# Performance work log

Hardware: AMD Instinct MI355X
Metric: run time of the kernel (lower is better)

The kernel has to match this reference:

```python
import jax, jax.numpy as jnp
import numpy as np

B, N, NSAMPLE = 8, 2048, 32
D = 64          # input feature channels
C1, C2 = 64, 128  # MLP channels (channels list after +3 on input: 67 -> 64 -> 128)
RADIUS = 0.15
EPS = 1e-5


def setup_inputs() -> dict:
    key = jax.random.key(0)
    ks = jax.random.split(key, 4)
    position = jax.random.uniform(ks[0], (B, N, 3), dtype=jnp.float32)
    feature = jax.random.normal(ks[1], (B, N, D), dtype=jnp.float32)
    W1 = jax.random.normal(ks[2], (D + 3, C1), dtype=jnp.float32) * 0.05
    gamma1 = jnp.ones((C1,), jnp.float32)
    beta1 = jnp.zeros((C1,), jnp.float32)
    W2 = jax.random.normal(ks[3], (C1, C2), dtype=jnp.float32) * 0.05
    gamma2 = jnp.ones((C2,), jnp.float32)
    beta2 = jnp.zeros((C2,), jnp.float32)
    return {"position": position, "feature": feature,
            "W1": W1, "gamma1": gamma1, "beta1": beta1,
            "W2": W2, "gamma2": gamma2, "beta2": beta2}


def _ball_query(xyz, radius, nsample):
    # squared pairwise distances [B, N, N]
    sq = (jnp.sum(xyz ** 2, -1)[:, :, None]
          + jnp.sum(xyz ** 2, -1)[:, None, :]
          - 2.0 * jnp.einsum('bnc,bmc->bnm', xyz, xyz))
    n = xyz.shape[1]
    idx = jnp.where(sq > radius ** 2, n, jnp.arange(n, dtype=jnp.int32)[None, None, :])
    idx = jnp.sort(idx, axis=-1)[:, :, :nsample]            # [B, N, nsample]
    first = idx[:, :, :1]
    return jnp.where(idx == n, first, idx)                  # pad misses with first neighbor


def _gather(points, idx):
    # points [B, N, C], idx [B, S, K] -> [B, S, K, C]
    b, s, k = idx.shape
    flat = jnp.take_along_axis(points, idx.reshape(b, s * k, 1), axis=1)
    return flat.reshape(b, s, k, points.shape[-1])


def _bn_relu(x, gamma, beta, relu=True):
    # BatchNorm1d over channel dim (train-mode stats across B*N*S), per linearblock
    mean = jnp.mean(x, axis=(0, 1, 2), keepdims=True)
    var = jnp.var(x, axis=(0, 1, 2), keepdims=True)
    y = (x - mean) * jax.lax.rsqrt(var + EPS) * gamma + beta
    return jax.nn.relu(y) if relu else y


def reference(position, feature, W1, gamma1, beta1, W2, gamma2, beta2):
    b, n, _ = position.shape
    idx = _ball_query(position, RADIUS, NSAMPLE)            # [B, N, nsample]
    grouped_xyz = _gather(position, idx) - position[:, :, None, :]  # [B,N,ns,3]
    grouped_feat = _gather(feature, idx)                    # [B, N, ns, D]
    h = jnp.concatenate([grouped_xyz, grouped_feat], axis=-1)  # [B, N, ns, 3+D]
    h = _bn_relu(h @ W1, gamma1, beta1)                     # [B, N, ns, C1]
    h = _bn_relu(h @ W2, gamma2, beta2)                     # [B, N, ns, C2]
    new_feature = jnp.max(h, axis=2)                        # [B, N, C2]
    return position, new_feature
```

## Files before the change

kernel.cpp:

```cpp
#include <hip/hip_runtime.h>
#include <hip/hip_bf16.h>


#define BB 8
#define NN 2048
#define KK 32
#define DD 64
#define CC1 64
#define CC2 128
#define TOTROWS (BB*NN*KK)
#define SITES (BB*NN)
#define PSLICES 256
#define DBLOCKS 1024

typedef __bf16 bf16x8 __attribute__((ext_vector_type(8)));
typedef float  f32x4  __attribute__((ext_vector_type(4)));

__device__ __forceinline__ void lds_add(float* p, float v) {
  __hip_atomic_fetch_add(p, v, __ATOMIC_RELAXED, __HIP_MEMORY_SCOPE_WORKGROUP);
}

__global__ __launch_bounds__(1024, 1) void kQ_ball_scatter(
    const float* __restrict__ pos, int* __restrict__ idx,
    float* __restrict__ Pc, float* __restrict__ Px,
    float* __restrict__ Py, float* __restrict__ Pz,
    float* __restrict__ momP, float* __restrict__ out)
{
  __shared__ float4 P[NN];
  __shared__ unsigned int Sc[NN], Sx[NN], Sy[NN], Sz[NN];
  __shared__ int idxL[64*KK];
  __shared__ float mred[16*9];
  const int b = blockIdx.x >> 5;
  const int slice = blockIdx.x & 31;
  for (int i = threadIdx.x; i < NN; i += 1024) {
    const float* p = pos + ((size_t)b*NN + i)*3;
    float x = p[0], y = p[1], z = p[2];
    float s = __fadd_rn(__fadd_rn(__fmul_rn(x,x), __fmul_rn(y,y)), __fmul_rn(z,z));
    P[i] = make_float4(x, y, z, s);
    Sc[i] = 0u; Sx[i] = 0u; Sy[i] = 0u; Sz[i] = 0u;
  }
  __syncthreads();
  const int wave = threadIdx.x >> 6, lane = threadIdx.x & 63;
  const float R2 = (float)(0.15 * 0.15);
  const unsigned long long lt = (lane == 63) ? 0x7fffffffffffffffull
                                             : ((1ull << lane) - 1ull);
  for (int qi = wave; qi < 64; qi += 16) {
    const int q = slice*64 + qi;
    const float4 Q = P[q];
    int* ip = idx + ((size_t)b*NN + q)*KK;
    int* il = idxL + qi*KK;
    int cnt = 0, first = -1;
    for (int step = 0; step < 32; ++step) {
      float4 p = P[step*64 + lane];
      float d = __fmul_rn(Q.x, p.x);
      d = fmaf(Q.y, p.y, d);
      d = fmaf(Q.z, p.z, d);
      float sq = __fsub_rn(__fadd_rn(Q.w, p.w), __fmul_rn(2.0f, d));
      bool in = !(sq > R2);
      unsigned long long mask = __ballot(in);
      if (first < 0 && mask) first = step*64 + (int)__builtin_ctzll(mask);
      int dst = cnt + (int)__popcll(mask & lt);
      if (in && dst < KK) { ip[dst] = step*64 + lane; il[dst] = step*64 + lane; }
      cnt += (int)__popcll(mask);
      if (cnt >= KK) break;
    }
    if (lane >= cnt && lane < KK) { ip[lane] = first; il[lane] = first; }
  }
  __syncthreads();
  const int sl = threadIdx.x >> 4;
  const int kg = threadIdx.x & 15;
  const int ip0 = idxL[sl*KK];
  const float4 C = P[slice*64 + sl];
  const float FS = 4194304.0f;
  float m1x=0.f,m1y=0.f,m1z=0.f,mxx=0.f,myy=0.f,mzz=0.f,mxy=0.f,mxz=0.f,myz=0.f;
  int wt = 0;
  #pragma unroll
  for (int j = 0; j < 2; ++j) {
    const int k = kg*2 + j;
    const int m = idxL[sl*KK + k];
    const float4 Pm = P[m];
    float dx = Pm.x - C.x;
    float dy = Pm.y - C.y;
    float dz = Pm.z - C.z;
    if (k > 0 && m == ip0) {
      ++wt;
    } else {
      atomicAdd(&Sc[m], 1u);
      atomicAdd(&Sx[m], (unsigned int)__float2int_rn(dx*FS));
      atomicAdd(&Sy[m], (unsigned int)__float2int_rn(dy*FS));
      atomicAdd(&Sz[m], (unsigned int)__float2int_rn(dz*FS));
    }
    m1x += dx; m1y += dy; m1z += dz;
    mxx = fmaf(dx,dx,mxx); myy = fmaf(dy,dy,myy); mzz = fmaf(dz,dz,mzz);
    mxy = fmaf(dx,dy,mxy); mxz = fmaf(dx,dz,mxz); myz = fmaf(dy,dz,myz);
  }
  if (wt > 0) {
    const float4 P0 = P[ip0];
    float dx0 = P0.x - C.x;
    float dy0 = P0.y - C.y;
    float dz0 = P0.z - C.z;
    atomicAdd(&Sc[ip0], (unsigned int)wt);
    atomicAdd(&Sx[ip0], (unsigned int)(wt*__float2int_rn(dx0*FS)));
    atomicAdd(&Sy[ip0], (unsigned int)(wt*__float2int_rn(dy0*FS)));
    atomicAdd(&Sz[ip0], (unsigned int)(wt*__float2int_rn(dz0*FS)));
  }
  const int wv = threadIdx.x >> 6;
  float vals[9] = {m1x,m1y,m1z,mxx,myy,mzz,mxy,mxz,myz};
  #pragma unroll
  for (int i = 0; i < 9; ++i) {
    float v = vals[i];
    #pragma unroll
    for (int s = 1; s < 64; s <<= 1) v += __shfl_xor(v, s, 64);
    if (lane == 0) mred[wv*9 + i] = v;
  }
  __syncthreads();
  const float IS = 2.38418579101562500e-7f;
  float* pc = Pc + (size_t)blockIdx.x*NN;
  float* px = Px + (size_t)blockIdx.x*NN;
  float* py = Py + (size_t)blockIdx.x*NN;
  float* pz = Pz + (size_t)blockIdx.x*NN;
  for (int i = threadIdx.x; i < NN; i += 1024) {
    pc[i] = (float)Sc[i];
    px[i] = (float)(int)Sx[i] * IS;
    py[i] = (float)(int)Sy[i] * IS;
    pz[i] = (float)(int)Sz[i] * IS;
  }
  if (threadIdx.x < 9) {
    float s = 0.f;
    #pragma unroll
    for (int w2 = 0; w2 < 16; ++w2) s += mred[w2*9 + threadIdx.x];
    momP[(size_t)blockIdx.x*16 + threadIdx.x] = s;
  }
  if (threadIdx.x < 192)
    out[blockIdx.x*192 + threadIdx.x] = pos[blockIdx.x*192 + threadIdx.x];
}

__global__ __launch_bounds__(256) void kB_g(const float* __restrict__ feat,
                                            const float* __restrict__ W1,
                                            const float* __restrict__ Pc,
                                            const float* __restrict__ Px,
                                            const float* __restrict__ Py,
                                            const float* __restrict__ Pz,
                                            float* __restrict__ g,
                                            float* __restrict__ A_p)
{
  __shared__ float red[320];
  __shared__ float cntL[128], dxL[128], dyL[128], dzL[128];
  for (int i = threadIdx.x; i < 320; i += 256) red[i] = 0.f;
  const int row0B = blockIdx.x * 128;
  const int bb = row0B >> 11;
  for (int r2 = threadIdx.x; r2 < 128; r2 += 256) {
    const int m = (row0B + r2) & (NN-1);
    float s0 = 0.f, s1 = 0.f, s2 = 0.f, s3 = 0.f;
    #pragma unroll 4
    for (int q = 0; q < 32; ++q) {
      const size_t base = (size_t)(bb*32 + q)*NN + m;
      s0 += Pc[base]; s1 += Px[base]; s2 += Py[base]; s3 += Pz[base];
    }
    cntL[r2] = s0; dxL[r2] = s1; dyL[r2] = s2; dzL[r2] = s3;
  }
  __syncthreads();
  const int lane = threadIdx.x & 63;
  const int quad = lane >> 4;
  const int col  = lane & 15;
  const int gw = (blockIdx.x*256 + threadIdx.x) >> 6;

  bf16x8 Bf[2][4];
  #pragma unroll
  for (int kt = 0; kt < 2; ++kt)
    #pragma unroll
    for (int nt = 0; nt < 4; ++nt) {
      bf16x8 v;
      #pragma unroll
      for (int j = 0; j < 8; ++j)
        v[j] = (__bf16)W1[(3 + kt*32 + quad*8 + j)*CC1 + nt*16 + col];
      Bf[kt][nt] = v;
    }
  float a1[4], a2[4], a3[4], a4[4], a5[4];
  #pragma unroll
  for (int nt = 0; nt < 4; ++nt) { a1[nt]=0.f; a2[nt]=0.f; a3[nt]=0.f; a4[nt]=0.f; a5[nt]=0.f; }

  for (int t = 0; t < 2; ++t) {
    const int row0 = (gw*2 + t) * 16;
    bf16x8 Af[2];
    #pragma unroll
    for (int kt = 0; kt < 2; ++kt) {
      const float4* fp =
        (const float4*)(feat + (size_t)(row0 + col)*DD + kt*32 + quad*8);
      float4 f0 = fp[0], f1 = fp[1];
      float fv[8] = {f0.x,f0.y,f0.z,f0.w,f1.x,f1.y,f1.z,f1.w};
      bf16x8 v;
      #pragma unroll
      for (int j = 0; j < 8; ++j) v[j] = (__bf16)fv[j];
      Af[kt] = v;
    }
    float cw[4], dxw[4], dyw[4], dzw[4];
    #pragma unroll
    for (int r = 0; r < 4; ++r) {
      int rl = row0 - row0B + quad*4 + r;
      cw[r] = cntL[rl]; dxw[r] = dxL[rl]; dyw[r] = dyL[rl]; dzw[r] = dzL[rl];
    }
    #pragma unroll
    for (int nt = 0; nt < 4; ++nt) {
      f32x4 a = {0.f, 0.f, 0.f, 0.f};
      a = __builtin_amdgcn_mfma_f32_16x16x32_bf16(Af[0], Bf[0][nt], a, 0, 0, 0);
      a = __builtin_amdgcn_mfma_f32_16x16x32_bf16(Af[1], Bf[1][nt], a, 0, 0, 0);
      #pragma unroll
      for (int r = 0; r < 4; ++r) {
        float v = a[r];
        g[(size_t)(row0 + quad*4 + r)*CC1 + nt*16 + col] = v;
        float cv = cw[r]*v;
        a1[nt] += cv; a2[nt] = fmaf(cv, v, a2[nt]);
        a3[nt] = fmaf(dxw[r], v, a3[nt]);
        a4[nt] = fmaf(dyw[r], v, a4[nt]);
        a5[nt] = fmaf(dzw[r], v, a5[nt]);
      }
    }
  }
  #pragma unroll
  for (int nt = 0; nt < 4; ++nt) {
    float v1=a1[nt], v2=a2[nt], v3=a3[nt], v4=a4[nt], v5=a5[nt];
    v1 += __shfl_xor(v1,16,64); v1 += __shfl_xor(v1,32,64);
    v2 += __shfl_xor(v2,16,64); v2 += __shfl_xor(v2,32,64);
    v3 += __shfl_xor(v3,16,64); v3 += __shfl_xor(v3,32,64);
    v4 += __shfl_xor(v4,16,64); v4 += __shfl_xor(v4,32,64);
    v5 += __shfl_xor(v5,16,64); v5 += __shfl_xor(v5,32,64);
    if (quad == 0) {
      int ch = nt*16 + col;
      lds_add(&red[ch], v1);
      lds_add(&red[64+ch], v2);
      lds_add(&red[128+ch], v3);
      lds_add(&red[192+ch], v4);
      lds_add(&red[256+ch], v5);
    }
  }
  __syncthreads();
  for (int i = threadIdx.x; i < 320; i += 256)
    A_p[(size_t)blockIdx.x*320 + i] = red[i];
}

__global__ __launch_bounds__(256) void kS_fold(
    const float* __restrict__ W1, const float* __restrict__ gamma1,
    const float* __restrict__ beta1, const float* __restrict__ A_p,
    const float* __restrict__ momP,
    float* __restrict__ sc1, float* __restrict__ sh1, float* __restrict__ W1s)
{
  __shared__ float AL[320];
  __shared__ float mr[256];
  __shared__ float momL[16];
  {
    const int t = threadIdx.x;
    const int i = t & 15, jq = t >> 4;
    float s = 0.f;
    #pragma unroll
    for (int q = 0; q < 16; ++q) s += momP[(size_t)(jq*16 + q)*16 + i];
    mr[t] = s;
  }
  for (int c = threadIdx.x; c < 320; c += 256) {
    float s = 0.f;
    for (int blk = 0; blk < 128; ++blk) s += A_p[(size_t)blk*320 + c];
    AL[c] = s;
  }
  __syncthreads();
  if (threadIdx.x < 16) {
    float tot = 0.f;
    #pragma unroll
    for (int q = 0; q < 16; ++q) tot += mr[q*16 + threadIdx.x];
    momL[threadIdx.x] = tot;
  }
  __syncthreads();
  const int c = threadIdx.x;
  if (c >= CC1) return;
  float wx = W1[c], wy = W1[CC1+c], wz = W1[2*CC1+c];
  float A1 = AL[c], A2 = AL[64+c];
  float A3x = AL[128+c], A3y = AL[192+c], A3z = AL[256+c];
  float sum1 = A1 + wx*momL[0] + wy*momL[1] + wz*momL[2];
  float ss = A2 + 2.f*(wx*A3x + wy*A3y + wz*A3z)
           + wx*wx*momL[3] + wy*wy*momL[4] + wz*wz*momL[5]
           + 2.f*(wx*wy*momL[6] + wx*wz*momL[7] + wy*wz*momL[8]);
  const float invN = 1.0f / (float)TOTROWS;
  float mean = sum1 * invN;
  float var  = ss * invN - mean*mean;
  float sc = rsqrtf(var + 1e-5f) * gamma1[c];
  float sh = beta1[c] - mean * sc;
  sc1[c] = sc; sh1[c] = sh;
  W1s[c] = wx*sc; W1s[64+c] = wy*sc; W1s[128+c] = wz*sc;
}

__global__ __launch_bounds__(256, 2) void kD_mfma(
    const float* __restrict__ pos, const int* __restrict__ idx,
    const float* __restrict__ g, const float* __restrict__ sc1,
    const float* __restrict__ sh1, const float* __restrict__ W1s,
    const float* __restrict__ W2,
    float* __restrict__ stats2P, float* __restrict__ out_nf)
{
  __shared__ __bf16 W2T[CC2*72];
  __shared__ float red2[256];
  red2[threadIdx.x] = 0.f;
  {
    const int n  = threadIdx.x & 127;
    const int k0 = (threadIdx.x >> 7) << 5;
    #pragma unroll
    for (int jj = 0; jj < 4; ++jj) {
      unsigned int pk[4];
      #pragma unroll
      for (int q2 = 0; q2 < 4; ++q2) {
        const int k = k0 + jj*8 + q2*2;
        __bf16 lo = (__bf16)W2[(size_t)k*CC2 + n];
        __bf16 hi = (__bf16)W2[(size_t)(k+1)*CC2 + n];
        unsigned short ulo, uhi;
        __builtin_memcpy(&ulo, &lo, 2);
        __builtin_memcpy(&uhi, &hi, 2);
        pk[q2] = ((unsigned int)uhi << 16) | (unsigned int)ulo;
      }
      __builtin_memcpy(&W2T[n*72 + k0 + jj*8], pk, 16);
    }
  }
  __syncthreads();

  const int lane = threadIdx.x & 63;
  const int quad = lane >> 4;
  const int col  = lane & 15;
  const int wv = (blockIdx.x*256 + threadIdx.x) >> 6;

  float ssum[8], ssq[8];
  #pragma unroll
  for (int nt = 0; nt < 8; ++nt) { ssum[nt] = 0.f; ssq[nt] = 0.f; }

  #pragma clang loop unroll(disable)
  for (int si = 0; si < 4; ++si) {
    const int site = wv*4 + si;
    const int b  = site >> 11;
    const int ls = site & (NN-1);
    const float* pb = pos + (size_t)b*NN*3;
    const int* ip = idx + (size_t)site*KK;

    const int ma = ip[col], mb = ip[16 + col];
    const float ccx = pb[ls*3], ccy = pb[ls*3+1], ccz = pb[ls*3+2];
    const float dxa = pb[ma*3]-ccx, dya = pb[ma*3+1]-ccy, dza = pb[ma*3+2]-ccz;
    const float dxb = pb[mb*3]-ccx, dyb = pb[mb*3+1]-ccy, dzb = pb[mb*3+2]-ccz;

    const float* gbase = g + (size_t)b*NN*CC1;
    const float* ra = gbase + (size_t)ma*CC1 + quad*8;
    const float* rb = gbase + (size_t)mb*CC1 + quad*8;
    f32x4 gA0 = *(const f32x4*)ra,      gA1 = *(const f32x4*)(ra+4);
    f32x4 gA2 = *(const f32x4*)(ra+32), gA3 = *(const f32x4*)(ra+36);
    f32x4 gB0 = *(const f32x4*)rb,      gB1 = *(const f32x4*)(rb+4);
    f32x4 gB2 = *(const f32x4*)(rb+32), gB3 = *(const f32x4*)(rb+36);

    bf16x8 A00, A01, A10, A11;
    {
      const int c0 = quad*8;
      f32x4 x0 = *(const f32x4*)&W1s[c0],     x1 = *(const f32x4*)&W1s[c0+4];
      f32x4 y0 = *(const f32x4*)&W1s[64+c0],  y1 = *(const f32x4*)&W1s[64+c0+4];
      f32x4 z0 = *(const f32x4*)&W1s[128+c0], z1 = *(const f32x4*)&W1s[128+c0+4];
      f32x4 s0 = *(const f32x4*)&sc1[c0],     s1 = *(const f32x4*)&sc1[c0+4];
      f32x4 h0 = *(const f32x4*)&sh1[c0],     h1 = *(const f32x4*)&sh1[c0+4];
      #pragma unroll
      for (int j = 0; j < 8; ++j) {
        float wx = (j<4)?x0[j]:x1[j-4], wy = (j<4)?y0[j]:y1[j-4];
        float wz = (j<4)?z0[j]:z1[j-4], sc = (j<4)?s0[j]:s1[j-4];
        float sh = (j<4)?h0[j]:h1[j-4];
        float ga = (j<4)?gA0[j]:gA1[j-4], gb = (j<4)?gB0[j]:gB1[j-4];
        float ta = fmaf(dza, wz, fmaf(dya, wy, fmaf(dxa, wx, sh)));
        A00[j] = (__bf16)fmaxf(fmaf(ga, sc, ta), 0.f);
        float tb = fmaf(dzb, wz, fmaf(dyb, wy, fmaf(dxb, wx, sh)));
        A10[j] = (__bf16)fmaxf(fmaf(gb, sc, tb), 0.f);
      }
    }
    {
      const int c0 = 32 + quad*8;
      f32x4 x0 = *(const f32x4*)&W1s[c0],     x1 = *(const f32x4*)&W1s[c0+4];
      f32x4 y0 = *(const f32x4*)&W1s[64+c0],  y1 = *(const f32x4*)&W1s[64+c0+4];
      f32x4 z0 = *(const f32x4*)&W1s[128+c0], z1 = *(const f32x4*)&W1s[128+c0+4];
      f32x4 s0 = *(const f32x4*)&sc1[c0],     s1 = *(const f32x4*)&sc1[c0+4];
      f32x4 h0 = *(const f32x4*)&sh1[c0],     h1 = *(const f32x4*)&sh1[c0+4];
      #pragma unroll
      for (int j = 0; j < 8; ++j) {
        float wx = (j<4)?x0[j]:x1[j-4], wy = (j<4)?y0[j]:y1[j-4];
        float wz = (j<4)?z0[j]:z1[j-4], sc = (j<4)?s0[j]:s1[j-4];
        float sh = (j<4)?h0[j]:h1[j-4];
        float ga = (j<4)?gA2[j]:gA3[j-4], gb = (j<4)?gB2[j]:gB3[j-4];
        float ta = fmaf(dza, wz, fmaf(dya, wy, fmaf(dxa, wx, sh)));
        A01[j] = (__bf16)fmaxf(fmaf(ga, sc, ta), 0.f);
        float tb = fmaf(dzb, wz, fmaf(dyb, wy, fmaf(dxb, wx, sh)));
        A11[j] = (__bf16)fmaxf(fmaf(gb, sc, tb), 0.f);
      }
    }

    float* outp = out_nf + (size_t)site*CC2;
    #pragma unroll
    for (int nt = 0; nt < 8; ++nt) {
      const bf16x8 B0 = *(const bf16x8*)&W2T[(nt*16 + col)*72 + quad*8];
      const bf16x8 B1 = *(const bf16x8*)&W2T[(nt*16 + col)*72 + 32 + quad*8];
      float mxv = -3.0e38f;
      f32x4 a = {0.f, 0.f, 0.f, 0.f};
      a = __builtin_amdgcn_mfma_f32_16x16x32_bf16(A00, B0, a, 0, 0, 0);
      a = __builtin_amdgcn_mfma_f32_16x16x32_bf16(A01, B1, a, 0, 0, 0);
      #pragma unroll
      for (int r = 0; r < 4; ++r) {
        float v = a[r];
        ssum[nt] += v; ssq[nt] = fmaf(v, v, ssq[nt]); mxv = fmaxf(mxv, v);
      }
      f32x4 a2 = {0.f, 0.f, 0.f, 0.f};
      a2 = __builtin_amdgcn_mfma_f32_16x16x32_bf16(A10, B0, a2, 0, 0, 0);
      a2 = __builtin_amdgcn_mfma_f32_16x16x32_bf16(A11, B1, a2, 0, 0, 0);
      #pragma unroll
      for (int r = 0; r < 4; ++r) {
        float v = a2[r];
        ssum[nt] += v; ssq[nt] = fmaf(v, v, ssq[nt]); mxv = fmaxf(mxv, v);
      }
      mxv = fmaxf(mxv, __shfl_xor(mxv, 16, 64));
      mxv = fmaxf(mxv, __shfl_xor(mxv, 32, 64));
      if ((nt & 3) == quad) outp[nt*16 + col] = mxv;
    }
  }

  #pragma unroll
  for (int nt = 0; nt < 8; ++nt) {
    float s = ssum[nt];
    s += __shfl_xor(s, 16, 64); s += __shfl_xor(s, 32, 64);
    float q = ssq[nt];
    q += __shfl_xor(q, 16, 64); q += __shfl_xor(q, 32, 64);
    if (lane < 16) {
      atomicAdd(&red2[nt*16 + col], s);
      atomicAdd(&red2[128 + nt*16 + col], q);
    }
  }
  __syncthreads();
  stats2P[(size_t)blockIdx.x*256 + threadIdx.x] = red2[threadIdx.x];
}

__global__ __launch_bounds__(256) void k45_epi(
    const float* __restrict__ stats2P, const float* __restrict__ g2,
    const float* __restrict__ be2, float* __restrict__ out)
{
  __shared__ float stF[256];
  __shared__ float scL[128], shL[128];
  const int t = threadIdx.x;
  {
    float s = 0.f;
    for (int blk = 0; blk < DBLOCKS; ++blk)
      s += stats2P[(size_t)blk*256 + t];
    stF[t] = s;
  }
  __syncthreads();
  if (t < CC2) {
    const float invc = 1.0f / (float)TOTROWS;
    float mean = stF[t] * invc;
    float var  = stF[128 + t] * invc - mean*mean;
    float sc = rsqrtf(var + 1e-5f) * g2[t];
    scL[t] = sc; shL[t] = be2[t] - mean * sc;
  }
  __syncthreads();
  float* out_nf = out + (size_t)BB*NN*3;
  float4* o4 = (float4*)out_nf;
  const size_t e0 = (size_t)blockIdx.x * 2048;
  for (int e = t; e < 2048; e += 256) {
    float4 x = o4[e0 + e];
    const int c = (e << 2) & (CC2-1);
    x.x = fmaxf(fmaf(x.x, scL[c  ], shL[c  ]), 0.f);
    x.y = fmaxf(fmaf(x.y, scL[c+1], shL[c+1]), 0.f);
    x.z = fmaxf(fmaf(x.z, scL[c+2], shL[c+2]), 0.f);
    x.w = fmaxf(fmaf(x.w, scL[c+3], shL[c+3]), 0.f);
    o4[e0 + e] = x;
  }
}

extern "C" void kernel_launch(void* const* d_in, const int* in_sizes, int n_in,
                              void* d_out, int out_size, void* d_ws, size_t ws_size,
                              hipStream_t stream) {
  const float* pos  = (const float*)d_in[0];
  const float* feat = (const float*)d_in[1];
  const float* W1   = (const float*)d_in[2];
  const float* g1   = (const float*)d_in[3];
  const float* be1  = (const float*)d_in[4];
  const float* W2   = (const float*)d_in[5];
  const float* g2   = (const float*)d_in[6];
  const float* be2  = (const float*)d_in[7];
  float* out = (float*)d_out;
  float* out_nf = out + (size_t)BB*NN*3;

  char* w = (char*)d_ws;
  int*   idx    = (int*)w;
  float* sc1    = (float*)(w + 0x200000);
  float* sh1    = sc1 + 64;
  float* W1s    = sh1 + 64;
  float* A_p    = (float*)(w + 0x210000);
  float* momP   = (float*)(w + 0x250000);
  float* Pc     = (float*)(w + 0x260000);
  float* Px     = Pc + (size_t)PSLICES*NN;
  float* Py     = Px + (size_t)PSLICES*NN;
  float* Pz     = Py + (size_t)PSLICES*NN;
  float* stats2P= (float*)(w + 0x660000);
  float* g      = (float*)(w + 0xA60000);

  kQ_ball_scatter<<<256, 1024, 0, stream>>>(pos, idx, Pc, Px, Py, Pz, momP, out);
  kB_g      <<<128, 256, 0, stream>>>(feat, W1, Pc, Px, Py, Pz, g, A_p);
  kS_fold   <<<1, 256, 0, stream>>>(W1, g1, be1, A_p, momP, sc1, sh1, W1s);
  kD_mfma   <<<DBLOCKS, 256, 0, stream>>>(pos, idx, g, sc1, sh1, W1s, W2,
                                          stats2P, out_nf);
  k45_epi   <<<256, 256, 0, stream>>>(stats2P, g2, be2, out);
}
```

Baseline: 195.0 us.

## Split ball-query over more blocks and hoist BN2 stat reduction into own kernel

The ball-query/scatter kernel now handles 32 query points per block across 512 blocks instead of 64 across 256, with one neighbor per thread. This doubles the partial-scatter slices that kB_g must sum. The per-block redundant reduction of 1024 stats2P partials in the epilogue is moved into a separate 256-block reduction kernel, and the epilogue now uses 512 smaller blocks. The aim is more parallelism on the first and last stages, paid for with doubled position preloading per block, more partial-slice traffic, and an extra launch.

```diff
diff --git a/kernel.cpp b/kernel.cpp
--- a/kernel.cpp
+++ b/kernel.cpp
@@ -10,7 +10,7 @@
 #define CC2 128
 #define TOTROWS (BB*NN*KK)
 #define SITES (BB*NN)
-#define PSLICES 256
+#define PSLICES 512
 #define DBLOCKS 1024
 
 typedef __bf16 bf16x8 __attribute__((ext_vector_type(8)));
@@ -20,7 +20,7 @@
   __hip_atomic_fetch_add(p, v, __ATOMIC_RELAXED, __HIP_MEMORY_SCOPE_WORKGROUP);
 }
 
-__global__ __launch_bounds__(1024, 1) void kQ_ball_scatter(
+__global__ __launch_bounds__(1024, 8) void kQ_ball_scatter(
     const float* __restrict__ pos, int* __restrict__ idx,
     float* __restrict__ Pc, float* __restrict__ Px,
     float* __restrict__ Py, float* __restrict__ Pz,
@@ -28,10 +28,10 @@
 {
   __shared__ float4 P[NN];
   __shared__ unsigned int Sc[NN], Sx[NN], Sy[NN], Sz[NN];
-  __shared__ int idxL[64*KK];
+  __shared__ int idxL[32*KK];
   __shared__ float mred[16*9];
-  const int b = blockIdx.x >> 5;
-  const int slice = blockIdx.x & 31;
+  const int b = blockIdx.x >> 6;
+  const int slice = blockIdx.x & 63;
   for (int i = threadIdx.x; i < NN; i += 1024) {
     const float* p = pos + ((size_t)b*NN + i)*3;
     float x = p[0], y = p[1], z = p[2];
@@ -44,8 +44,8 @@
   const float R2 = (float)(0.15 * 0.15);
   const unsigned long long lt = (lane == 63) ? 0x7fffffffffffffffull
                                              : ((1ull << lane) - 1ull);
-  for (int qi = wave; qi < 64; qi += 16) {
-    const int q = slice*64 + qi;
+  for (int qi = wave; qi < 32; qi += 16) {
+    const int q = slice*32 + qi;
     const float4 Q = P[q];
     int* ip = idx + ((size_t)b*NN + q)*KK;
     int* il = idxL + qi*KK;
@@ -67,51 +67,29 @@
     if (lane >= cnt && lane < KK) { ip[lane] = first; il[lane] = first; }
   }
   __syncthreads();
-  const int sl = threadIdx.x >> 4;
-  const int kg = threadIdx.x & 15;
-  const int ip0 = idxL[sl*KK];
-  const float4 C = P[slice*64 + sl];
+  const int sl = threadIdx.x >> 5;
+  const int kg = threadIdx.x & 31;
+  const int m = idxL[sl*KK + kg];
+  const float4 C = P[slice*32 + sl];
+  const float4 Pm = P[m];
   const float FS = 4194304.0f;
-  float m1x=0.f,m1y=0.f,m1z=0.f,mxx=0.f,myy=0.f,mzz=0.f,mxy=0.f,mxz=0.f,myz=0.f;
-  int wt = 0;
-  #pragma unroll
-  for (int j = 0; j < 2; ++j) {
-    const int k = kg*2 + j;
-    const int m = idxL[sl*KK + k];
-    const float4 Pm = P[m];
+  {
     float dx = Pm.x - C.x;
     float dy = Pm.y - C.y;
     float dz = Pm.z - C.z;
-    if (k > 0 && m == ip0) {
-      ++wt;
-    } else {
-      atomicAdd(&Sc[m], 1u);
-      atomicAdd(&Sx[m], (unsigned int)__float2int_rn(dx*FS));
-      atomicAdd(&Sy[m], (unsigned int)__float2int_rn(dy*FS));
-      atomicAdd(&Sz[m], (unsigned int)__float2int_rn(dz*FS));
-    }
-    m1x += dx; m1y += dy; m1z += dz;
-    mxx = fmaf(dx,dx,mxx); myy = fmaf(dy,dy,myy); mzz = fmaf(dz,dz,mzz);
-    mxy = fmaf(dx,dy,mxy); mxz = fmaf(dx,dz,mxz); myz = fmaf(dy,dz,myz);
-  }
-  if (wt > 0) {
-    const float4 P0 = P[ip0];
-    float dx0 = P0.x - C.x;
-    float dy0 = P0.y - C.y;
-    float dz0 = P0.z - C.z;
-    atomicAdd(&Sc[ip0], (unsigned int)wt);
-    atomicAdd(&Sx[ip0], (unsigned int)(wt*__float2int_rn(dx0*FS)));
-    atomicAdd(&Sy[ip0], (unsigned int)(wt*__float2int_rn(dy0*FS)));
-    atomicAdd(&Sz[ip0], (unsigned int)(wt*__float2int_rn(dz0*FS)));
-  }
-  const int wv = threadIdx.x >> 6;
-  float vals[9] = {m1x,m1y,m1z,mxx,myy,mzz,mxy,mxz,myz};
-  #pragma unroll
-  for (int i = 0; i < 9; ++i) {
-    float v = vals[i];
-    #pragma unroll
-    for (int s = 1; s < 64; s <<= 1) v += __shfl_xor(v, s, 64);
-    if (lane == 0) mred[wv*9 + i] = v;
+    atomicAdd(&Sc[m], 1u);
+    atomicAdd(&Sx[m], (unsigned int)__float2int_rn(dx*FS));
+    atomicAdd(&Sy[m], (unsigned int)__float2int_rn(dy*FS));
+    atomicAdd(&Sz[m], (unsigned int)__float2int_rn(dz*FS));
+    float vals[9] = {dx, dy, dz, dx*dx, dy*dy, dz*dz, dx*dy, dx*dz, dy*dz};
+    const int wv = threadIdx.x >> 6;
+    #pragma unroll
+    for (int i = 0; i < 9; ++i) {
+      float v = vals[i];
+      #pragma unroll
+      for (int s = 1; s < 64; s <<= 1) v += __shfl_xor(v, s, 64);
+      if (lane == 0) mred[wv*9 + i] = v;
+    }
   }
   __syncthreads();
   const float IS = 2.38418579101562500e-7f;
@@ -131,8 +109,8 @@
     for (int w2 = 0; w2 < 16; ++w2) s += mred[w2*9 + threadIdx.x];
     momP[(size_t)blockIdx.x*16 + threadIdx.x] = s;
   }
-  if (threadIdx.x < 192)
-    out[blockIdx.x*192 + threadIdx.x] = pos[blockIdx.x*192 + threadIdx.x];
+  if (threadIdx.x < 96)
+    out[blockIdx.x*96 + threadIdx.x] = pos[blockIdx.x*96 + threadIdx.x];
 }
 
 __global__ __launch_bounds__(256) void kB_g(const float* __restrict__ feat,
@@ -153,8 +131,8 @@
     const int m = (row0B + r2) & (NN-1);
     float s0 = 0.f, s1 = 0.f, s2 = 0.f, s3 = 0.f;
     #pragma unroll 4
-    for (int q = 0; q < 32; ++q) {
-      const size_t base = (size_t)(bb*32 + q)*NN + m;
+    for (int q = 0; q < 64; ++q) {
+      const size_t base = (size_t)(bb*64 + q)*NN + m;
       s0 += Pc[base]; s1 += Px[base]; s2 += Py[base]; s3 += Pz[base];
     }
     cntL[r2] = s0; dxL[r2] = s1; dyL[r2] = s2; dzL[r2] = s3;
@@ -253,7 +231,7 @@
     const int i = t & 15, jq = t >> 4;
     float s = 0.f;
     #pragma unroll
-    for (int q = 0; q < 16; ++q) s += momP[(size_t)(jq*16 + q)*16 + i];
+    for (int q = 0; q < 32; ++q) s += momP[(size_t)(jq*32 + q)*16 + i];
     mr[t] = s;
   }
   for (int c = threadIdx.x; c < 320; c += 256) {
@@ -431,34 +409,43 @@
   stats2P[(size_t)blockIdx.x*256 + threadIdx.x] = red2[threadIdx.x];
 }
 
+__global__ __launch_bounds__(256) void kR2_stats(
+    const float* __restrict__ stats2P, float* __restrict__ stats2)
+{
+  __shared__ float r[256];
+  const int c = blockIdx.x;
+  float s = 0.f;
+  for (int i = threadIdx.x; i < DBLOCKS; i += 256)
+    s += stats2P[(size_t)i*256 + c];
+  r[threadIdx.x] = s;
+  __syncthreads();
+  for (int off = 128; off > 0; off >>= 1) {
+    if (threadIdx.x < off) r[threadIdx.x] += r[threadIdx.x + off];
+    __syncthreads();
+  }
+  if (threadIdx.x == 0) stats2[c] = r[0];
+}
+
 __global__ __launch_bounds__(256) void k45_epi(
-    const float* __restrict__ stats2P, const float* __restrict__ g2,
+    const float* __restrict__ stats2, const float* __restrict__ g2,
     const float* __restrict__ be2, float* __restrict__ out)
 {
-  __shared__ float stF[256];
   __shared__ float scL[128], shL[128];
   const int t = threadIdx.x;
-  {
-    float s = 0.f;
-    for (int blk = 0; blk < DBLOCKS; ++blk)
-      s += stats2P[(size_t)blk*256 + t];
-    stF[t] = s;
-  }
-  __syncthreads();
   if (t < CC2) {
     const float invc = 1.0f / (float)TOTROWS;
-    float mean = stF[t] * invc;
-    float var  = stF[128 + t] * invc - mean*mean;
+    float mean = stats2[t] * invc;
+    float var  = stats2[128 + t] * invc - mean*mean;
     float sc = rsqrtf(var + 1e-5f) * g2[t];
     scL[t] = sc; shL[t] = be2[t] - mean * sc;
   }
   __syncthreads();
   float* out_nf = out + (size_t)BB*NN*3;
   float4* o4 = (float4*)out_nf;
-  const size_t e0 = (size_t)blockIdx.x * 2048;
-  for (int e = t; e < 2048; e += 256) {
+  const size_t e0 = (size_t)blockIdx.x * 1024;
+  for (int e = t; e < 1024; e += 256) {
     float4 x = o4[e0 + e];
-    const int c = (e << 2) & (CC2-1);
+    const int c = (int)(((e0 + e) << 2) & (CC2-1));
     x.x = fmaxf(fmaf(x.x, scL[c  ], shL[c  ]), 0.f);
     x.y = fmaxf(fmaf(x.y, scL[c+1], shL[c+1]), 0.f);
     x.z = fmaxf(fmaf(x.z, scL[c+2], shL[c+2]), 0.f);
@@ -483,7 +470,8 @@
 
   char* w = (char*)d_ws;
   int*   idx    = (int*)w;
-  float* sc1    = (float*)(w + 0x200000);
+  float* stats2 = (float*)(w + 0x200000);
+  float* sc1    = stats2 + 256;
   float* sh1    = sc1 + 64;
   float* W1s    = sh1 + 64;
   float* A_p    = (float*)(w + 0x210000);
@@ -492,13 +480,14 @@
   float* Px     = Pc + (size_t)PSLICES*NN;
   float* Py     = Px + (size_t)PSLICES*NN;
   float* Pz     = Py + (size_t)PSLICES*NN;
-  float* stats2P= (float*)(w + 0x660000);
-  float* g      = (float*)(w + 0xA60000);
-
-  kQ_ball_scatter<<<256, 1024, 0, stream>>>(pos, idx, Pc, Px, Py, Pz, momP, out);
+  float* stats2P= (float*)(w + 0x1260000);
+  float* g      = (float*)(w + 0x1360000);
+
+  kQ_ball_scatter<<<512, 1024, 0, stream>>>(pos, idx, Pc, Px, Py, Pz, momP, out);
   kB_g      <<<128, 256, 0, stream>>>(feat, W1, Pc, Px, Py, Pz, g, A_p);
   kS_fold   <<<1, 256, 0, stream>>>(W1, g1, be1, A_p, momP, sc1, sh1, W1s);
   kD_mfma   <<<DBLOCKS, 256, 0, stream>>>(pos, idx, g, sc1, sh1, W1s, W2,
                                           stats2P, out_nf);
-  k45_epi   <<<256, 256, 0, stream>>>(stats2P, g2, be2, out);
-}
+  kR2_stats <<<256, 256, 0, stream>>>(stats2P, stats2);
+  k45_epi   <<<512, 256, 0, stream>>>(stats2, g2, be2, out);
+}
```

Result: faster. 178.0 us (-8.7%).
